# Performance work log

Measured on AMD Instinct MI355X. Metric: run time of the kernel, lower is better.

## Reference

```python
import jax, jax.numpy as jnp
import numpy as np

N_NODES = 100000
N_GRAPHS = 128

def _graph_conv(x, W, b, s, d, n_nodes):
    """DGL GraphConv with norm='both': D_dst^{-1/2} A D_src^{-1/2} X W + b."""
    ones = jnp.ones(s.shape[0], x.dtype)
    deg_out = jax.ops.segment_sum(ones, s, num_segments=n_nodes)  # src out-degree
    deg_in = jax.ops.segment_sum(ones, d, num_segments=n_nodes)   # dst in-degree
    norm_src = jnp.where(deg_out > 0, 1.0 / jnp.sqrt(jnp.maximum(deg_out, 1.0)), 0.0)
    norm_dst = jnp.where(deg_in > 0, 1.0 / jnp.sqrt(jnp.maximum(deg_in, 1.0)), 0.0)
    h = x * norm_src[:, None]                    # [N, F]
    agg = jax.ops.segment_sum(h[s], d, num_segments=n_nodes)  # SpMM gather-scatter
    rst = (agg @ W) * norm_dst[:, None] + b
    return rst

def _hetero_layer(x, Ws, bs, src, dst, n_nodes):
    # HeteroGraphConv aggregate='sum' over relations (fixed small set -> loop ok)
    out = jnp.zeros((n_nodes, Ws.shape[-1]), x.dtype)
    for r in range(Ws.shape[0]):
        out = out + _graph_conv(x, Ws[r], bs[r], src[r], dst[r], n_nodes)
    return out

def setup_inputs() -> dict:
    key = jax.random.key(0)
    ks = jax.random.split(key, 8)
    feat = jax.random.normal(ks[0], (N_NODES, 256), dtype=jnp.float32)
    src = jax.random.randint(ks[1], (3, 400000), 0, N_NODES)
    dst = jax.random.randint(ks[2], (3, 400000), 0, N_NODES)
    graph_ids = jnp.sort(jax.random.randint(ks[3], (N_NODES,), 0, N_GRAPHS))
    W1 = jax.random.normal(ks[4], (3, 256, 256), dtype=jnp.float32) * 0.06
    b1 = jnp.zeros((3, 256), dtype=jnp.float32)
    W2 = jax.random.normal(ks[5], (3, 256, 256), dtype=jnp.float32) * 0.06
    b2 = jnp.zeros((3, 256), dtype=jnp.float32)
    return {"feat": feat, "src": src, "dst": dst, "graph_ids": graph_ids,
            "W1": W1, "b1": b1, "W2": W2, "b2": b2}

def reference(feat, src, dst, graph_ids, W1, b1, W2, b2):
    n_nodes = feat.shape[0]
    h = _hetero_layer(feat, W1, b1, src, dst, n_nodes)
    h = jax.nn.relu(h)
    h = _hetero_layer(h, W2, b2, src, dst, n_nodes)
    # AvgPooling over batched graphs
    sums = jax.ops.segment_sum(h, graph_ids, num_segments=N_GRAPHS)
    counts = jax.ops.segment_sum(jnp.ones(n_nodes, h.dtype), graph_ids, num_segments=N_GRAPHS)
    return sums / jnp.maximum(counts, 1.0)[:, None]
```

## Files before the change

kernel.cpp:

```cpp
#include <hip/hip_runtime.h>
#include <stdint.h>

#define NN 100000
#define NE 400000
#define NR 3
#define NF 256
#define NK 768
#define NG 128
#define SCAN_NB ((NN + 1023) / 1024)

typedef __attribute__((ext_vector_type(4))) unsigned short ushortx4;
typedef __attribute__((ext_vector_type(8))) short short8;
typedef __attribute__((ext_vector_type(4))) float floatx4;

static __device__ __forceinline__ unsigned short f2bfu(float f) {
  union { float f; uint32_t u; } c; c.f = f;
  uint32_t x = c.u;
  uint32_t r = (x + 0x7fffu + ((x >> 16) & 1u)) >> 16;
  return (unsigned short)r;
}
static __device__ __forceinline__ float bfu2f(unsigned short u) {
  union { uint32_t u; float f; } c; c.u = ((uint32_t)u) << 16;
  return c.f;
}

static __device__ __forceinline__ void gload16(const void* g, void* l) {
  __builtin_amdgcn_global_load_lds(
      (const __attribute__((address_space(1))) uint32_t*)g,
      (__attribute__((address_space(3))) uint32_t*)l, 16, 0, 0);
}


__global__ __launch_bounds__(256) void degree_kernel(
    const int* __restrict__ src, const int* __restrict__ dst,
    int* __restrict__ deg_out, int* __restrict__ deg_in) {
  int t = blockIdx.x * 256 + threadIdx.x;
  int r = blockIdx.y;
  if (t < NE) {
    atomicAdd(&deg_out[r * NN + src[r * NE + t]], 1);
    atomicAdd(&deg_in[r * NN + dst[r * NE + t]], 1);
  }
}

__global__ __launch_bounds__(128) void gcount_kernel(
    const int* __restrict__ gid, int* __restrict__ gcount) {
  int g = threadIdx.x;
  int lo = 0, hi = NN;
  while (lo < hi) { int mid = (lo + hi) >> 1; if (gid[mid] < g) lo = mid + 1; else hi = mid; }
  int a = lo;
  lo = 0; hi = NN;
  while (lo < hi) { int mid = (lo + hi) >> 1; if (gid[mid] < g + 1) lo = mid + 1; else hi = mid; }
  gcount[g] = lo - a;
}

__global__ __launch_bounds__(256) void norm_kernel(
    const int* __restrict__ deg_out, const int* __restrict__ deg_in,
    float* __restrict__ n_src, float* __restrict__ n_dst) {
  int t = blockIdx.x * 256 + threadIdx.x;
  if (t < NR * NN) {
    int dof = deg_out[t], din = deg_in[t];
    n_src[t] = dof > 0 ? rsqrtf((float)dof) : 0.f;
    n_dst[t] = din > 0 ? rsqrtf((float)din) : 0.f;
  }
}


__global__ __launch_bounds__(256) void scan_phaseA(
    const int* __restrict__ deg_in, int* __restrict__ blocksum) {
  int r = blockIdx.y, b = blockIdx.x, tid = threadIdx.x;
  const int* deg = deg_in + (size_t)r * NN;
  int base = b * 1024 + tid * 4;
  int s = 0;
#pragma unroll
  for (int i = 0; i < 4; ++i) { int idx = base + i; if (idx < NN) s += deg[idx]; }
  __shared__ int red[256];
  red[tid] = s; __syncthreads();
  for (int off = 128; off > 0; off >>= 1) {
    if (tid < off) red[tid] += red[tid + off];
    __syncthreads();
  }
  if (tid == 0) blocksum[r * SCAN_NB + b] = red[0];
}

__global__ __launch_bounds__(128) void scan_phaseB(
    int* __restrict__ blocksum, int* __restrict__ rowptr) {
  int r = blockIdx.x, tid = threadIdx.x;
  int* bs = blocksum + r * SCAN_NB;
  __shared__ int buf[128];
  int v = (tid < SCAN_NB) ? bs[tid] : 0;
  buf[tid] = v; __syncthreads();
  for (int off = 1; off < 128; off <<= 1) {
    int t = (tid >= off) ? buf[tid - off] : 0;
    __syncthreads();
    buf[tid] += t;
    __syncthreads();
  }
  if (tid < SCAN_NB) bs[tid] = buf[tid] - v;
  if (tid == 127) rowptr[(size_t)r * (NN + 1) + NN] = buf[127];
}

__global__ __launch_bounds__(256) void scan_phaseC(
    const int* __restrict__ deg_in, const int* __restrict__ blocksum,
    int* __restrict__ rowptr) {
  int r = blockIdx.y, b = blockIdx.x, tid = threadIdx.x;
  const int* deg = deg_in + (size_t)r * NN;
  int* rp = rowptr + (size_t)r * (NN + 1);
  int base = b * 1024 + tid * 4;
  int v[4]; int s = 0;
#pragma unroll
  for (int i = 0; i < 4; ++i) { int idx = base + i; v[i] = (idx < NN) ? deg[idx] : 0; s += v[i]; }
  __shared__ int buf[256];
  buf[tid] = s; __syncthreads();
  for (int off = 1; off < 256; off <<= 1) {
    int t = (tid >= off) ? buf[tid - off] : 0;
    __syncthreads();
    buf[tid] += t;
    __syncthreads();
  }
  int excl = buf[tid] - s + blocksum[r * SCAN_NB + b];
#pragma unroll
  for (int i = 0; i < 4; ++i) {
    int idx = base + i;
    if (idx < NN) rp[idx] = excl;
    excl += v[i];
  }
}

__global__ __launch_bounds__(256) void scatter_kernel(
    const int* __restrict__ src, const int* __restrict__ dst,
    const int* __restrict__ rowptr, int* __restrict__ cursor,
    const float* __restrict__ n_src,
    int* __restrict__ csr_src, float* __restrict__ csr_w) {
  int t = blockIdx.x * 256 + threadIdx.x;
  int r = blockIdx.y;
  if (t < NE) {
    int s = src[r * NE + t], v = dst[r * NE + t];
    int pos = atomicAdd(&cursor[r * NN + v], 1);
    int idx = r * NE + rowptr[(size_t)r * (NN + 1) + v] + pos;
    csr_src[idx] = s;
    csr_w[idx] = n_src[r * NN + s];
  }
}


__global__ __launch_bounds__(256) void prep_w_kernel(
    const float* __restrict__ W1, const float* __restrict__ W2,
    unsigned short* __restrict__ wt1, unsigned short* __restrict__ wt2) {
  int t = blockIdx.x * 256 + threadIdx.x;
  int lay = t / (NR * NF * NF);
  int rem = t % (NR * NF * NF);
  int r = rem / (NF * NF);
  int k = (rem / NF) % NF;
  int n = rem % NF;
  const float* W = lay ? W2 : W1;
  unsigned short* wt = lay ? wt2 : wt1;
  wt[(size_t)n * NK + r * NF + k] = f2bfu(W[((size_t)r * NF + k) * NF + n]);
}

__global__ __launch_bounds__(256) void prep_bias_kernel(
    const float* __restrict__ b1, const float* __restrict__ b2,
    float* __restrict__ bs1, float* __restrict__ bs2) {
  int t = blockIdx.x * 256 + threadIdx.x;
  if (t < 2 * NF) {
    int lay = t / NF, n = t % NF;
    const float* b = lay ? b2 : b1;
    float* bs = lay ? bs2 : bs1;
    bs[n] = b[n] + b[NF + n] + b[2 * NF + n];
  }
}

__global__ __launch_bounds__(256) void cast_kernel(
    const float* __restrict__ in, unsigned short* __restrict__ out, int n4) {
  int t = blockIdx.x * 256 + threadIdx.x;
  if (t < n4) {
    floatx4 v = *(const floatx4*)&in[(size_t)t * 4];
    ushortx4 o;
    o.x = f2bfu(v.x); o.y = f2bfu(v.y); o.z = f2bfu(v.z); o.w = f2bfu(v.w);
    *(ushortx4*)&out[(size_t)t * 4] = o;
  }
}


__global__ __launch_bounds__(256) void spmm_kernel(
    const unsigned short* __restrict__ x,
    const int* __restrict__ rowptr, const int* __restrict__ csr_src,
    const float* __restrict__ csr_w, const float* __restrict__ n_dst,
    unsigned short* __restrict__ agg) {
  int wid = threadIdx.x >> 6, l = threadIdx.x & 63;
  int r = blockIdx.y;
  int v = blockIdx.x * 4 + wid;
  if (v >= NN) return;
  int e0 = rowptr[(size_t)r * (NN + 1) + v];
  int e1 = rowptr[(size_t)r * (NN + 1) + v + 1];
  const int* cs = csr_src + (size_t)r * NE;
  const float* cw = csr_w + (size_t)r * NE;
  float a0 = 0.f, a1 = 0.f, a2 = 0.f, a3 = 0.f;
  for (int e = e0; e < e1; ++e) {
    int s = cs[e];
    float w = cw[e];
    ushortx4 xv = *(const ushortx4*)&x[(size_t)s * NF + l * 4];
    a0 += w * bfu2f(xv.x);
    a1 += w * bfu2f(xv.y);
    a2 += w * bfu2f(xv.z);
    a3 += w * bfu2f(xv.w);
  }
  float nd = n_dst[r * NN + v];
  ushortx4 o;
  o.x = f2bfu(a0 * nd); o.y = f2bfu(a1 * nd);
  o.z = f2bfu(a2 * nd); o.w = f2bfu(a3 * nd);
  *(ushortx4*)&agg[(size_t)v * NK + r * NF + l * 4] = o;
}


__global__ __launch_bounds__(256) void gemm_kernel(
    const unsigned short* __restrict__ A,
    const unsigned short* __restrict__ Bt,
    const float* __restrict__ bias,
    unsigned short* __restrict__ C,
    int M, int relu) {
  __shared__ unsigned short ldsA[128 * 32];
  __shared__ unsigned short ldsB[128 * 32];
  const int tid = threadIdx.x;
  const int l = tid & 63, wid = tid >> 6;
  const int wr = wid >> 1, wc = wid & 1;
  const int row0 = blockIdx.x * 128, col0 = blockIdx.y * 128;

  floatx4 acc[4][4];
#pragma unroll
  for (int i = 0; i < 4; ++i)
#pragma unroll
    for (int j = 0; j < 4; ++j)
#pragma unroll
      for (int q = 0; q < 4; ++q) acc[i][j][q] = 0.f;

  const int srow = l >> 2;
  const int skc = (l & 3) * 8;
  const int fr = l & 15, fk = (l >> 4) * 8;

  for (int kt = 0; kt < NK / 32; ++kt) {
    const int k0 = kt * 32;
#pragma unroll
    for (int it = 0; it < 2; ++it) {
      int ci = it * 4 + wid;
      int arow = row0 + ci * 16 + srow;
      if (arow >= M) arow = M - 1;
      gload16(A + (size_t)arow * NK + k0 + skc, &ldsA[ci * 512 + l * 8]);
      int brow = col0 + ci * 16 + srow;
      gload16(Bt + (size_t)brow * NK + k0 + skc, &ldsB[ci * 512 + l * 8]);
    }
    asm volatile("s_waitcnt vmcnt(0)" ::: "memory");
    __syncthreads();

    short8 af[4], bf[4];
#pragma unroll
    for (int m = 0; m < 4; ++m)
      af[m] = *(const short8*)&ldsA[(wr * 64 + m * 16 + fr) * 32 + fk];
#pragma unroll
    for (int n = 0; n < 4; ++n)
      bf[n] = *(const short8*)&ldsB[(wc * 64 + n * 16 + fr) * 32 + fk];
#pragma unroll
    for (int m = 0; m < 4; ++m)
#pragma unroll
      for (int n = 0; n < 4; ++n)
        acc[m][n] = __builtin_amdgcn_mfma_f32_16x16x32_bf16(af[m], bf[n], acc[m][n], 0, 0, 0);
    __syncthreads();
  }

  const int fq = l >> 4;
#pragma unroll
  for (int m = 0; m < 4; ++m) {
#pragma unroll
    for (int n = 0; n < 4; ++n) {
      int col = col0 + wc * 64 + n * 16 + fr;
      float bv = bias[col];
#pragma unroll
      for (int q = 0; q < 4; ++q) {
        int row = row0 + wr * 64 + m * 16 + fq * 4 + q;
        if (row < M) {
          float vv = acc[m][n][q] + bv;
          if (relu) vv = fmaxf(vv, 0.f);
          C[(size_t)row * NF + col] = f2bfu(vv);
        }
      }
    }
  }
}


__global__ __launch_bounds__(256) void pool_kernel(
    const unsigned short* __restrict__ h2, const int* __restrict__ gid,
    float* __restrict__ poolsum) {
  int c = threadIdx.x;
  int v0 = blockIdx.x * 256;
  int vend = min(v0 + 256, NN);
  float acc = 0.f;
  int curg = -1;
  for (int v = v0; v < vend; ++v) {
    int g = gid[v];
    if (g != curg) {
      if (curg >= 0) atomicAdd(&poolsum[curg * NF + c], acc);
      curg = g; acc = 0.f;
    }
    acc += bfu2f(h2[(size_t)v * NF + c]);
  }
  if (curg >= 0) atomicAdd(&poolsum[curg * NF + c], acc);
}

__global__ __launch_bounds__(256) void final_kernel(
    const float* __restrict__ poolsum, const int* __restrict__ gcount,
    float* __restrict__ out) {
  int g = blockIdx.x, c = threadIdx.x;
  out[g * NF + c] = poolsum[g * NF + c] / fmaxf((float)gcount[g], 1.f);
}


extern "C" void kernel_launch(void* const* d_in, const int* in_sizes, int n_in,
                              void* d_out, int out_size, void* d_ws, size_t ws_size,
                              hipStream_t stream) {
  const float* feat = (const float*)d_in[0];
  const int* src = (const int*)d_in[1];
  const int* dst = (const int*)d_in[2];
  const int* gid = (const int*)d_in[3];
  const float* W1 = (const float*)d_in[4];
  const float* b1 = (const float*)d_in[5];
  const float* W2 = (const float*)d_in[6];
  const float* b2 = (const float*)d_in[7];
  float* out = (float*)d_out;

  char* ws = (char*)d_ws;
  size_t off = 0;
  auto alloc = [&](size_t bytes) -> void* {
    void* p = ws + off;
    off = (off + bytes + 255) & ~(size_t)255;
    return p;
  };

  int* deg_out = (int*)alloc((size_t)NR * NN * 4);
  int* deg_in  = (int*)alloc((size_t)NR * NN * 4);
  int* cursor  = (int*)alloc((size_t)NR * NN * 4);
  float* poolsum = (float*)alloc((size_t)NG * NF * 4);
  size_t zero_bytes = off;

  int* gcount  = (int*)alloc((size_t)NG * 4);
  int* blocksum = (int*)alloc((size_t)NR * SCAN_NB * 4);
  float* n_src = (float*)alloc((size_t)NR * NN * 4);
  float* n_dst = (float*)alloc((size_t)NR * NN * 4);
  int* rowptr  = (int*)alloc((size_t)NR * (NN + 1) * 4);
  int* csr_src = (int*)alloc((size_t)NR * NE * 4);
  float* csr_w = (float*)alloc((size_t)NR * NE * 4);
  unsigned short* wt1 = (unsigned short*)alloc((size_t)NF * NK * 2);
  unsigned short* wt2 = (unsigned short*)alloc((size_t)NF * NK * 2);
  float* bs1 = (float*)alloc(NF * 4);
  float* bs2 = (float*)alloc(NF * 4);
  unsigned short* featbf = (unsigned short*)alloc((size_t)NN * NF * 2);
  unsigned short* h1 = (unsigned short*)alloc((size_t)NN * NF * 2);
  unsigned short* h2 = (unsigned short*)alloc((size_t)NN * NF * 2);
  unsigned short* agg = (unsigned short*)alloc((size_t)NN * NK * 2);
  (void)ws_size; (void)in_sizes; (void)n_in; (void)out_size;

  hipMemsetAsync(d_ws, 0, zero_bytes, stream);

  dim3 eg((NE + 255) / 256, NR);
  degree_kernel<<<eg, 256, 0, stream>>>(src, dst, deg_out, deg_in);
  gcount_kernel<<<1, 128, 0, stream>>>(gid, gcount);
  norm_kernel<<<(NR * NN + 255) / 256, 256, 0, stream>>>(deg_out, deg_in, n_src, n_dst);
  scan_phaseA<<<dim3(SCAN_NB, NR), 256, 0, stream>>>(deg_in, blocksum);
  scan_phaseB<<<NR, 128, 0, stream>>>(blocksum, rowptr);
  scan_phaseC<<<dim3(SCAN_NB, NR), 256, 0, stream>>>(deg_in, blocksum, rowptr);
  scatter_kernel<<<eg, 256, 0, stream>>>(src, dst, rowptr, cursor, n_src, csr_src, csr_w);

  prep_w_kernel<<<(2 * NR * NF * NF) / 256, 256, 0, stream>>>(W1, W2, wt1, wt2);
  prep_bias_kernel<<<2, 256, 0, stream>>>(b1, b2, bs1, bs2);
  cast_kernel<<<(NN * NF / 4 + 255) / 256, 256, 0, stream>>>(feat, featbf, NN * NF / 4);

  dim3 sg((NN + 3) / 4, NR);
  spmm_kernel<<<sg, 256, 0, stream>>>(featbf, rowptr, csr_src, csr_w, n_dst, agg);
  gemm_kernel<<<dim3((NN + 127) / 128, 2), 256, 0, stream>>>(agg, wt1, bs1, h1, NN, 1);
  spmm_kernel<<<sg, 256, 0, stream>>>(h1, rowptr, csr_src, csr_w, n_dst, agg);
  gemm_kernel<<<dim3((NN + 127) / 128, 2), 256, 0, stream>>>(agg, wt2, bs2, h2, NN, 0);
  pool_kernel<<<(NN + 255) / 256, 256, 0, stream>>>(h2, gid, poolsum);
  final_kernel<<<NG, 256, 0, stream>>>(poolsum, gcount, out);
}
```

Before: 841.5 us.

## Unroll SpMM edge loop by four and widen GEMM tile to full 256 columns

The SpMM inner loop is unrolled by four so that four independent neighbour-row gathers are in flight at once, hiding gather latency. The GEMM now has each block compute a 128x256 tile covering all output columns, with each wave doing 128x64. This means the A tile (the 768-wide aggregated features) is read from global memory once instead of twice. The cost is more accumulator registers per wave (32 MFMA tiles), a launch bound that caps occupancy at 2 blocks, and twice the LDS for B.

```diff
diff --git a/kernel.cpp b/kernel.cpp
--- a/kernel.cpp
+++ b/kernel.cpp
@@ -195,7 +195,20 @@
   const int* cs = csr_src + (size_t)r * NE;
   const float* cw = csr_w + (size_t)r * NE;
   float a0 = 0.f, a1 = 0.f, a2 = 0.f, a3 = 0.f;
-  for (int e = e0; e < e1; ++e) {
+  int e = e0;
+  for (; e + 4 <= e1; e += 4) {
+    int s0 = cs[e], s1 = cs[e + 1], s2 = cs[e + 2], s3 = cs[e + 3];
+    float w0 = cw[e], w1 = cw[e + 1], w2 = cw[e + 2], w3 = cw[e + 3];
+    ushortx4 x0 = *(const ushortx4*)&x[(size_t)s0 * NF + l * 4];
+    ushortx4 x1 = *(const ushortx4*)&x[(size_t)s1 * NF + l * 4];
+    ushortx4 x2 = *(const ushortx4*)&x[(size_t)s2 * NF + l * 4];
+    ushortx4 x3 = *(const ushortx4*)&x[(size_t)s3 * NF + l * 4];
+    a0 += w0 * bfu2f(x0.x) + w1 * bfu2f(x1.x) + w2 * bfu2f(x2.x) + w3 * bfu2f(x3.x);
+    a1 += w0 * bfu2f(x0.y) + w1 * bfu2f(x1.y) + w2 * bfu2f(x2.y) + w3 * bfu2f(x3.y);
+    a2 += w0 * bfu2f(x0.z) + w1 * bfu2f(x1.z) + w2 * bfu2f(x2.z) + w3 * bfu2f(x3.z);
+    a3 += w0 * bfu2f(x0.w) + w1 * bfu2f(x1.w) + w2 * bfu2f(x2.w) + w3 * bfu2f(x3.w);
+  }
+  for (; e < e1; ++e) {
     int s = cs[e];
     float w = cw[e];
     ushortx4 xv = *(const ushortx4*)&x[(size_t)s * NF + l * 4];
@@ -212,54 +225,59 @@
 }
 
 
-__global__ __launch_bounds__(256) void gemm_kernel(
+__global__ __launch_bounds__(256, 2) void gemm_kernel(
     const unsigned short* __restrict__ A,
     const unsigned short* __restrict__ Bt,
     const float* __restrict__ bias,
     unsigned short* __restrict__ C,
     int M, int relu) {
   __shared__ unsigned short ldsA[128 * 32];
-  __shared__ unsigned short ldsB[128 * 32];
+  __shared__ unsigned short ldsB[256 * 32];
   const int tid = threadIdx.x;
   const int l = tid & 63, wid = tid >> 6;
-  const int wr = wid >> 1, wc = wid & 1;
-  const int row0 = blockIdx.x * 128, col0 = blockIdx.y * 128;
-
-  floatx4 acc[4][4];
-#pragma unroll
-  for (int i = 0; i < 4; ++i)
+  const int row0 = blockIdx.x * 128;
+  const int c0 = wid * 64;
+
+  floatx4 acc[8][4];
+#pragma unroll
+  for (int i = 0; i < 8; ++i)
 #pragma unroll
     for (int j = 0; j < 4; ++j)
 #pragma unroll
       for (int q = 0; q < 4; ++q) acc[i][j][q] = 0.f;
 
-  const int srow = l >> 2;
-  const int skc = (l & 3) * 8;
   const int fr = l & 15, fk = (l >> 4) * 8;
 
   for (int kt = 0; kt < NK / 32; ++kt) {
     const int k0 = kt * 32;
-#pragma unroll
-    for (int it = 0; it < 2; ++it) {
-      int ci = it * 4 + wid;
-      int arow = row0 + ci * 16 + srow;
+    {
+      int u = wid * 64 + l;
+      int arow = row0 + (u >> 2);
       if (arow >= M) arow = M - 1;
-      gload16(A + (size_t)arow * NK + k0 + skc, &ldsA[ci * 512 + l * 8]);
-      int brow = col0 + ci * 16 + srow;
-      gload16(Bt + (size_t)brow * NK + k0 + skc, &ldsB[ci * 512 + l * 8]);
+      gload16(A + (size_t)arow * NK + k0 + (u & 3) * 8, &ldsA[u * 8]);
+      u += 256;
+      arow = row0 + (u >> 2);
+      if (arow >= M) arow = M - 1;
+      gload16(A + (size_t)arow * NK + k0 + (u & 3) * 8, &ldsA[u * 8]);
+    }
+#pragma unroll
+    for (int p = 0; p < 4; ++p) {
+      int u = p * 256 + wid * 64 + l;
+      int col = u >> 2;
+      gload16(Bt + (size_t)col * NK + k0 + (u & 3) * 8, &ldsB[u * 8]);
     }
     asm volatile("s_waitcnt vmcnt(0)" ::: "memory");
     __syncthreads();
 
-    short8 af[4], bf[4];
-#pragma unroll
-    for (int m = 0; m < 4; ++m)
-      af[m] = *(const short8*)&ldsA[(wr * 64 + m * 16 + fr) * 32 + fk];
+    short8 af[8], bf[4];
+#pragma unroll
+    for (int m = 0; m < 8; ++m)
+      af[m] = *(const short8*)&ldsA[(m * 16 + fr) * 32 + fk];
 #pragma unroll
     for (int n = 0; n < 4; ++n)
-      bf[n] = *(const short8*)&ldsB[(wc * 64 + n * 16 + fr) * 32 + fk];
-#pragma unroll
-    for (int m = 0; m < 4; ++m)
+      bf[n] = *(const short8*)&ldsB[(c0 + n * 16 + fr) * 32 + fk];
+#pragma unroll
+    for (int m = 0; m < 8; ++m)
 #pragma unroll
       for (int n = 0; n < 4; ++n)
         acc[m][n] = __builtin_amdgcn_mfma_f32_16x16x32_bf16(af[m], bf[n], acc[m][n], 0, 0, 0);
@@ -268,14 +286,14 @@
 
   const int fq = l >> 4;
 #pragma unroll
-  for (int m = 0; m < 4; ++m) {
+  for (int m = 0; m < 8; ++m) {
 #pragma unroll
     for (int n = 0; n < 4; ++n) {
-      int col = col0 + wc * 64 + n * 16 + fr;
+      int col = c0 + n * 16 + fr;
       float bv = bias[col];
 #pragma unroll
       for (int q = 0; q < 4; ++q) {
-        int row = row0 + wr * 64 + m * 16 + fq * 4 + q;
+        int row = row0 + m * 16 + fq * 4 + q;
         if (row < M) {
           float vv = acc[m][n][q] + bv;
           if (relu) vv = fmaxf(vv, 0.f);
@@ -375,9 +393,9 @@
 
   dim3 sg((NN + 3) / 4, NR);
   spmm_kernel<<<sg, 256, 0, stream>>>(featbf, rowptr, csr_src, csr_w, n_dst, agg);
-  gemm_kernel<<<dim3((NN + 127) / 128, 2), 256, 0, stream>>>(agg, wt1, bs1, h1, NN, 1);
+  gemm_kernel<<<(NN + 127) / 128, 256, 0, stream>>>(agg, wt1, bs1, h1, NN, 1);
   spmm_kernel<<<sg, 256, 0, stream>>>(h1, rowptr, csr_src, csr_w, n_dst, agg);
-  gemm_kernel<<<dim3((NN + 127) / 128, 2), 256, 0, stream>>>(agg, wt2, bs2, h2, NN, 0);
+  gemm_kernel<<<(NN + 127) / 128, 256, 0, stream>>>(agg, wt2, bs2, h2, NN, 0);
   pool_kernel<<<(NN + 255) / 256, 256, 0, stream>>>(h2, gid, poolsum);
   final_kernel<<<NG, 256, 0, stream>>>(poolsum, gcount, out);
 }
```

After: 740.0 us. 1.14x faster.
